# Optimization experiments

Hardware: AMD Instinct MI355X
Metric: run time of the kernel (lower is better)

Reference implementation:

```python
import jax, jax.numpy as jnp
import numpy as np

N = 50000          # num nodes
E = 800000         # num edges
H, C = 2, 64       # heads, per-head channels (hidden_dim=64)
IN_DIM = 128
EDGE_DIM = 32
NEG_SLOPE = 0.2


def setup_inputs() -> dict:
    key = jax.random.key(0)
    ks = jax.random.split(key, 20)
    s = 0.05
    inp = {
        'x': jax.random.normal(ks[0], (N, IN_DIM), jnp.float32),
        'edge_index': jax.random.randint(ks[1], (2, E), 0, N, jnp.int64),
        'edge_attr': jax.random.normal(ks[2], (E, EDGE_DIM), jnp.float32),
    }
    k = 3
    for l in range(3):
        inp[f'Wl{l}'] = jax.random.normal(ks[k], (IN_DIM, H * C), jnp.float32) * s; k += 1
        inp[f'Wr{l}'] = jax.random.normal(ks[k], (IN_DIM, H * C), jnp.float32) * s; k += 1
        inp[f'We{l}'] = jax.random.normal(ks[k], (EDGE_DIM, H * C), jnp.float32) * s; k += 1
        inp[f'att{l}'] = jax.random.normal(ks[k], (H, C), jnp.float32) * s; k += 1
        inp[f'b{l}'] = jnp.zeros((H * C,), jnp.float32)
    return inp


def gatv2_layer(x, src, dst, edge_attr, Wl, Wr, We, att, b):
    # PyG GATv2Conv (concat=True, share_weights=False):
    #   e_ij = att . LeakyReLU(Wl x_j + Wr x_i + We edge_ij)
    #   alpha = softmax_j over neighborhood of dst i; out_i = sum_j alpha_ij * (Wl x_j)
    xl = (x @ Wl).reshape(-1, H, C)              # [N,H,C] source transform
    xr = (x @ Wr).reshape(-1, H, C)              # [N,H,C] target transform
    ea = (edge_attr @ We).reshape(-1, H, C)      # [E,H,C]
    xj = xl[src]                                 # [E,H,C] gather source
    e = jax.nn.leaky_relu(xj + xr[dst] + ea, NEG_SLOPE)
    logits = jnp.einsum('ehc,hc->eh', e, att)    # [E,H]
    # segment softmax over dst neighborhoods
    m = jax.ops.segment_max(logits, dst, num_segments=N)  # [N,H]
    m = jnp.where(jnp.isfinite(m), m, 0.0)
    ex = jnp.exp(logits - m[dst])
    denom = jax.ops.segment_sum(ex, dst, num_segments=N)  # [N,H]
    alpha = ex / (denom[dst] + 1e-16)            # [E,H]
    out = jax.ops.segment_sum(alpha[:, :, None] * xj, dst, num_segments=N)  # [N,H,C]
    return out.reshape(-1, H * C) + b


def reference(x, edge_index, edge_attr,
              Wl0, Wr0, We0, att0, b0,
              Wl1, Wr1, We1, att1, b1,
              Wl2, Wr2, We2, att2, b2):
    src, dst = edge_index[0], edge_index[1]
    h = gatv2_layer(x, src, dst, edge_attr, Wl0, Wr0, We0, att0, b0)
    h = jax.nn.relu(h)
    h = gatv2_layer(h, src, dst, edge_attr, Wl1, Wr1, We1, att1, b1)
    h = jax.nn.relu(h)
    h = gatv2_layer(h, src, dst, edge_attr, Wl2, Wr2, We2, att2, b2)
    return h
```

## Files before the change

### kernel.cpp

```cpp
#include <hip/hip_runtime.h>

typedef unsigned int u32;
typedef unsigned short u16;
typedef __attribute__((ext_vector_type(8))) short bf16x8;
typedef __attribute__((ext_vector_type(4))) float f32x4;

__device__ __forceinline__ u16 f2b(float f){
  u32 x = __float_as_uint(f);
  u32 r = (x + 0x7fffu + ((x >> 16) & 1u)) >> 16;
  return (u16)r;
}
__device__ __forceinline__ float b2f(u16 h){ return __uint_as_float((u32)h << 16); }
__device__ __forceinline__ float bl(u32 u){ return __uint_as_float(u << 16); }
__device__ __forceinline__ float bh(u32 u){ return __uint_as_float(u & 0xffff0000u); }


__global__ void k_detect(const u32* __restrict__ ei, int n, u32* __restrict__ flag){
  int t = blockIdx.x * blockDim.x + threadIdx.x;
  u32 v = 0;
  if (t < n) v = ei[2 * t + 1];
  unsigned long long b = __ballot(v != 0u);
  if ((threadIdx.x & 63) == 0 && b) atomicOr(flag, 1u);
}

__global__ void k_convhist(const int* __restrict__ ei, int* __restrict__ src, int* __restrict__ dst,
                           int* __restrict__ deg, int E, const u32* __restrict__ flag){
  int e = blockIdx.x * blockDim.x + threadIdx.x;
  if (e >= E) return;
  bool is64 = (*flag == 0u);
  int s, d;
  if (is64){ s = ei[2 * e]; d = ei[2 * (E + e)]; }
  else     { s = ei[e];     d = ei[E + e]; }
  src[e] = s; dst[e] = d;
  atomicAdd(&deg[d], 1);
}

__global__ __launch_bounds__(256) void k_scan1(const int* __restrict__ deg, int* __restrict__ bsum, int n,
                                               int* __restrict__ ssrc, int* __restrict__ sdst,
                                               u16* __restrict__ ea2s_pad, int E){
  int b = blockIdx.x, t = threadIdx.x, lane = t & 63, wv = t >> 6;
  if (b == 0){
    if (t < 64){ ssrc[E + t] = 0; sdst[E + t] = 0; }
    ((uint4*)ea2s_pad)[t] = make_uint4(0, 0, 0, 0);
  }
  int i0 = b * 1024 + t * 4;
  int4 v = make_int4(0,0,0,0);
  if (i0 + 3 < n) v = *(const int4*)(deg + i0);
  else { if (i0 < n) v.x = deg[i0]; if (i0+1 < n) v.y = deg[i0+1]; if (i0+2 < n) v.z = deg[i0+2]; }
  int s = v.x + v.y + v.z + v.w;
  #pragma unroll
  for (int off = 1; off < 64; off <<= 1) s += __shfl_xor(s, off);
  __shared__ int ws[4];
  if (lane == 0) ws[wv] = s;
  __syncthreads();
  if (t == 0) bsum[b] = ws[0] + ws[1] + ws[2] + ws[3];
}

__global__ __launch_bounds__(1024) void k_scan2(int* __restrict__ bsum, int nb, int* __restrict__ segN){
  int t = threadIdx.x, lane = t & 63, w = t >> 6;
  int v = (t < nb) ? bsum[t] : 0;
  int x = v;
  #pragma unroll
  for (int off = 1; off < 64; off <<= 1){
    int y = __shfl_up(x, off);
    if (lane >= off) x += y;
  }
  __shared__ int wsum[16];
  if (lane == 63) wsum[w] = x;
  __syncthreads();
  if (w == 0 && lane < 16){
    int sv = wsum[lane];
    #pragma unroll
    for (int off = 1; off < 16; off <<= 1){
      int y = __shfl_up(sv, off);
      if (lane >= off) sv += y;
    }
    wsum[lane] = sv;
  }
  __syncthreads();
  int woff = (w > 0) ? wsum[w - 1] : 0;
  if (t < nb) bsum[t] = woff + x - v;
  if (t == 0) *segN = wsum[15];
}

__global__ __launch_bounds__(256) void k_scan3(const int* __restrict__ deg, const int* __restrict__ bsum,
                                               int* __restrict__ seg, int n){
  int b = blockIdx.x, t = threadIdx.x, lane = t & 63, wv = t >> 6;
  int i0 = b * 1024 + t * 4;
  int4 v = make_int4(0,0,0,0);
  if (i0 + 3 < n) v = *(const int4*)(deg + i0);
  else { if (i0 < n) v.x = deg[i0]; if (i0+1 < n) v.y = deg[i0+1]; if (i0+2 < n) v.z = deg[i0+2]; }
  int s = v.x + v.y + v.z + v.w;
  int x = s;
  #pragma unroll
  for (int off = 1; off < 64; off <<= 1){
    int y = __shfl_up(x, off);
    if (lane >= off) x += y;
  }
  __shared__ int ws[4];
  if (lane == 63) ws[wv] = x;
  __syncthreads();
  int woff = 0;
  #pragma unroll
  for (int k = 0; k < 4; k++) if (k < wv) woff += ws[k];
  int base = bsum[b] + woff + (x - s);
  if (i0 < n)     seg[i0]     = base;
  if (i0+1 < n)   seg[i0+1]   = base + v.x;
  if (i0+2 < n)   seg[i0+2]   = base + v.x + v.y;
  if (i0+3 < n)   seg[i0+3]   = base + v.x + v.y + v.z;
}

__global__ void k_scatter(const int* __restrict__ src, const int* __restrict__ dst,
                          const int* __restrict__ seg, int* __restrict__ cur,
                          int* __restrict__ ssrc, int* __restrict__ sdst,
                          int* __restrict__ seid, int E){
  int e = blockIdx.x * blockDim.x + threadIdx.x;
  if (e >= E) return;
  int d = dst[e];
  int pos = seg[d] + atomicAdd(&cur[d], 1);
  ssrc[pos] = src[e];
  sdst[pos] = d;
  seid[pos] = e;
}

__global__ void k_sortb(const int* __restrict__ seid, const float* __restrict__ eattr,
                        u16* __restrict__ ea2s, int E){
  int t = blockIdx.x * blockDim.x + threadIdx.x;
  int e = t >> 3, j = t & 7;
  if (e >= E) return;
  int eid = seid[e];
  float4 v = *(const float4*)(eattr + (size_t)eid * 32 + j * 4);
  u32 p0 = (u32)f2b(v.x) | ((u32)f2b(v.y) << 16);
  u32 p1 = (u32)f2b(v.z) | ((u32)f2b(v.w) << 16);
  *(uint2*)(ea2s + (size_t)e * 32 + j * 4) = make_uint2(p0, p1);
}

__global__ __launch_bounds__(256) void k_prepw(
    const float* __restrict__ W0, const float* __restrict__ W1, const float* __restrict__ W2,
    const float* __restrict__ W3, const float* __restrict__ W4, const float* __restrict__ W5,
    u16* __restrict__ WtH, u16* __restrict__ WtL)
{
  int mat = blockIdx.z;
  const float* W = (mat == 0) ? W0 : (mat == 1) ? W1 : (mat == 2) ? W2 :
                   (mat == 3) ? W3 : (mat == 4) ? W4 : W5;
  __shared__ float tile[32][33];
  int kt = blockIdx.x * 32, ct = blockIdx.y * 32;
  int tr = threadIdx.x & 31, ti = threadIdx.x >> 5;
  #pragma unroll
  for (int j = 0; j < 4; j++){
    int kk = ti + 8 * j;
    tile[kk][tr] = W[(size_t)(kt + kk) * 128 + ct + tr];
  }
  __syncthreads();
  #pragma unroll
  for (int j = 0; j < 4; j++){
    int cc = ti + 8 * j;
    float v = tile[tr][cc];
    u16 hi = f2b(v);
    u16 lo = f2b(v - b2f(hi));
    size_t o = (size_t)mat * 16384 + (size_t)(ct + cc) * 128 + kt + tr;
    WtH[o] = hi;
    WtL[o] = lo;
  }
}

__global__ __launch_bounds__(512) void k_gemm2(
    const float* __restrict__ A,
    const u16* __restrict__ WtH, const u16* __restrict__ WtL,
    u16* __restrict__ xlb, u16* __restrict__ xrb, int nrows)
{
  __shared__ u16 sAH[64][32], sAL[64][32];
  __shared__ u16 sWH[256][32], sWL[256][32];
  int t = threadIdx.x, wv = t >> 6, lane = t & 63;
  int col = lane & 15, kg = lane >> 4;
  int mat = wv >> 2, cq = wv & 3;
  int r0 = blockIdx.x * 64;

  f32x4 acc[4][2];
  #pragma unroll
  for (int m = 0; m < 4; m++)
    #pragma unroll
    for (int n = 0; n < 2; n++)
      acc[m][n] = (f32x4){0.f, 0.f, 0.f, 0.f};

  int ar = t >> 3, ak = (t & 7) << 2;
  int wmt = t >> 8, wtt = t & 255;
  int wc = wtt >> 1, wk = (wtt & 1) << 4;

  for (int kh = 0; kh < 4; kh++){
    __syncthreads();
    {
      int gr = r0 + ar;
      const float* ap = A + (size_t)gr * 128 + kh * 32 + ak;
      float4 va = {0,0,0,0};
      if (gr < nrows) va = *(const float4*)ap;
      u16 h0 = f2b(va.x), h1 = f2b(va.y), h2 = f2b(va.z), h3 = f2b(va.w);
      u16 l0 = f2b(va.x - b2f(h0)), l1 = f2b(va.y - b2f(h1));
      u16 l2 = f2b(va.z - b2f(h2)), l3 = f2b(va.w - b2f(h3));
      *(uint2*)&sAH[ar][ak] = make_uint2((u32)h0 | ((u32)h1 << 16), (u32)h2 | ((u32)h3 << 16));
      *(uint2*)&sAL[ar][ak] = make_uint2((u32)l0 | ((u32)l1 << 16), (u32)l2 | ((u32)l3 << 16));
    }
    {
      const u16* gh = WtH + (size_t)wmt * 16384 + (size_t)wc * 128 + kh * 32 + wk;
      const u16* gl = WtL + (size_t)wmt * 16384 + (size_t)wc * 128 + kh * 32 + wk;
      uint4 h0 = *(const uint4*)gh, h1 = *(const uint4*)(gh + 8);
      uint4 l0 = *(const uint4*)gl, l1 = *(const uint4*)(gl + 8);
      *(uint4*)&sWH[wmt * 128 + wc][wk]     = h0; *(uint4*)&sWH[wmt * 128 + wc][wk + 8] = h1;
      *(uint4*)&sWL[wmt * 128 + wc][wk]     = l0; *(uint4*)&sWL[wmt * 128 + wc][wk + 8] = l1;
    }
    __syncthreads();
    int wb = mat * 128 + cq * 32;
    bf16x8 bhi0 = *(const bf16x8*)&sWH[wb + col]     [kg*8];
    bf16x8 bhi1 = *(const bf16x8*)&sWH[wb + 16 + col][kg*8];
    bf16x8 blo0 = *(const bf16x8*)&sWL[wb + col]     [kg*8];
    bf16x8 blo1 = *(const bf16x8*)&sWL[wb + 16 + col][kg*8];
    #pragma unroll
    for (int m = 0; m < 4; m++){
      bf16x8 ahv = *(const bf16x8*)&sAH[m*16 + col][kg*8];
      bf16x8 alv = *(const bf16x8*)&sAL[m*16 + col][kg*8];
      acc[m][0] = __builtin_amdgcn_mfma_f32_16x16x32_bf16(ahv, bhi0, acc[m][0], 0, 0, 0);
      acc[m][0] = __builtin_amdgcn_mfma_f32_16x16x32_bf16(alv, bhi0, acc[m][0], 0, 0, 0);
      acc[m][0] = __builtin_amdgcn_mfma_f32_16x16x32_bf16(ahv, blo0, acc[m][0], 0, 0, 0);
      acc[m][1] = __builtin_amdgcn_mfma_f32_16x16x32_bf16(ahv, bhi1, acc[m][1], 0, 0, 0);
      acc[m][1] = __builtin_amdgcn_mfma_f32_16x16x32_bf16(alv, bhi1, acc[m][1], 0, 0, 0);
      acc[m][1] = __builtin_amdgcn_mfma_f32_16x16x32_bf16(ahv, blo1, acc[m][1], 0, 0, 0);
    }
  }
  u16* ob = mat ? xrb : xlb;
  #pragma unroll
  for (int m = 0; m < 4; m++){
    #pragma unroll
    for (int n = 0; n < 2; n++){
      #pragma unroll
      for (int r = 0; r < 4; r++){
        int row = r0 + m*16 + kg*4 + r;
        int c   = cq*32 + n*16 + col;
        if (row < nrows) ob[(size_t)row * 128 + c] = f2b(acc[m][n][r]);
      }
    }
  }
}

__global__ __launch_bounds__(256) void k_edge(
    const int* __restrict__ ssrc, const int* __restrict__ sdst,
    const u16* __restrict__ ea2s,
    const u16* __restrict__ xlb, const u16* __restrict__ xrb,
    const float* __restrict__ We, const float* __restrict__ att,
    float2* __restrict__ pr2, int ntiles, int E)
{
  __shared__ float sD[4][16][132];
  int wv = threadIdx.x >> 6, lane = threadIdx.x & 63;
  int col = lane & 15, kg = lane >> 4;
  int er = lane >> 2, q = lane & 3;

  bf16x8 bw[8];
  #pragma unroll
  for (int c = 0; c < 8; c++)
    #pragma unroll
    for (int j = 0; j < 8; j++)
      bw[c][j] = (short)f2b(We[(kg * 8 + j) * 128 + c * 16 + col]);
  u32 attp[16];
  #pragma unroll
  for (int i = 0; i < 16; i++)
    attp[i] = (u32)f2b(att[q * 32 + 2*i]) | ((u32)f2b(att[q * 32 + 2*i + 1]) << 16);

  int nw = gridDim.x * 4;
  int t = blockIdx.x * 4 + wv;
  if (t >= ntiles) return;

  int e0 = t * 16;
  int p = e0 + er;
  bf16x8 aA = *(const bf16x8*)(ea2s + (size_t)(e0 + col) * 32 + kg * 8);
  int snA = ssrc[p], dnA = sdst[p];
  const u16* xjA = xlb + (size_t)snA * 128 + q * 32;
  uint4 jA0 = ((const uint4*)xjA)[0], jA1 = ((const uint4*)xjA)[1],
        jA2 = ((const uint4*)xjA)[2], jA3 = ((const uint4*)xjA)[3];

  int tB = t + nw;
  int tBc = (tB < ntiles) ? tB : t;
  int eB = tBc * 16;
  int pB = eB + er;
  bf16x8 aB = *(const bf16x8*)(ea2s + (size_t)(eB + col) * 32 + kg * 8);
  int snB = ssrc[pB], dnB = sdst[pB];
  const u16* xjB = xlb + (size_t)snB * 128 + q * 32;
  uint4 jB0 = ((const uint4*)xjB)[0], jB1 = ((const uint4*)xjB)[1],
        jB2 = ((const uint4*)xjB)[2], jB3 = ((const uint4*)xjB)[3];

  while (true){
    const u16* xip = xrb + (size_t)dnA * 128 + q * 32;
    uint4 i0 = ((const uint4*)xip)[0], i1 = ((const uint4*)xip)[1],
          i2 = ((const uint4*)xip)[2], i3 = ((const uint4*)xip)[3];

    int tC = t + 2 * nw;
    int tCc = (tC < ntiles) ? tC : t;
    int eC = tCc * 16;
    int pC = eC + er;
    bf16x8 aC = *(const bf16x8*)(ea2s + (size_t)(eC + col) * 32 + kg * 8);
    int snC = ssrc[pC], dnC = sdst[pC];
    const u16* xjC = xlb + (size_t)snC * 128 + q * 32;
    uint4 jC0 = ((const uint4*)xjC)[0], jC1 = ((const uint4*)xjC)[1],
          jC2 = ((const uint4*)xjC)[2], jC3 = ((const uint4*)xjC)[3];

    #pragma unroll
    for (int c = 0; c < 8; c++){
      f32x4 d = __builtin_amdgcn_mfma_f32_16x16x32_bf16(aA, bw[c], (f32x4){0.f,0.f,0.f,0.f}, 0, 0, 0);
      #pragma unroll
      for (int r = 0; r < 4; r++)
        sD[wv][kg * 4 + r][c * 16 + col] = d[r];
    }

    const float* drow = &sD[wv][er][q * 32];
    float acc = 0.f;
#define EPK(KO, JQ, IQ) { \
    float4 d0 = *(const float4*)(drow + KO*8); \
    float4 d1 = *(const float4*)(drow + KO*8 + 4); \
    float v; u32 jw, iw, aw; \
    jw = JQ.x; iw = IQ.x; aw = attp[KO*4+0]; \
    v = d0.x + bl(jw) + bl(iw); v = fmaxf(v, 0.2f*v); acc = fmaf(v, bl(aw), acc); \
    v = d0.y + bh(jw) + bh(iw); v = fmaxf(v, 0.2f*v); acc = fmaf(v, bh(aw), acc); \
    jw = JQ.y; iw = IQ.y; aw = attp[KO*4+1]; \
    v = d0.z + bl(jw) + bl(iw); v = fmaxf(v, 0.2f*v); acc = fmaf(v, bl(aw), acc); \
    v = d0.w + bh(jw) + bh(iw); v = fmaxf(v, 0.2f*v); acc = fmaf(v, bh(aw), acc); \
    jw = JQ.z; iw = IQ.z; aw = attp[KO*4+2]; \
    v = d1.x + bl(jw) + bl(iw); v = fmaxf(v, 0.2f*v); acc = fmaf(v, bl(aw), acc); \
    v = d1.y + bh(jw) + bh(iw); v = fmaxf(v, 0.2f*v); acc = fmaf(v, bh(aw), acc); \
    jw = JQ.w; iw = IQ.w; aw = attp[KO*4+3]; \
    v = d1.z + bl(jw) + bl(iw); v = fmaxf(v, 0.2f*v); acc = fmaf(v, bl(aw), acc); \
    v = d1.w + bh(jw) + bh(iw); v = fmaxf(v, 0.2f*v); acc = fmaf(v, bh(aw), acc); }
    EPK(0, jA0, i0) EPK(1, jA1, i1) EPK(2, jA2, i2) EPK(3, jA3, i3)
#undef EPK
    acc += __shfl_xor(acc, 1);
    float other = __shfl_xor(acc, 2);
    if (q == 0 && p < E){
      pr2[p] = make_float2(__expf(fminf(acc, 80.f)), __expf(fminf(other, 80.f)));
    }
    int t2 = t + nw;
    if (t2 >= ntiles) break;
    t = t2; p = pB;
    aA = aB; dnA = dnB;
    jA0 = jB0; jA1 = jB1; jA2 = jB2; jA3 = jB3;
    aB = aC; dnB = dnC; pB = pC;
    jB0 = jC0; jB1 = jC1; jB2 = jC2; jB3 = jC3;
  }
}

template<int RELU>
__global__ __launch_bounds__(256) void k_seg2(
    const int* __restrict__ seg, const int* __restrict__ ssrc,
    const float2* __restrict__ pr2,
    const u16* __restrict__ xlb, const float* __restrict__ bias,
    float* __restrict__ out, int N)
{
  int wid  = blockIdx.x * 4 + (threadIdx.x >> 6);
  int lane = threadIdx.x & 63;
  if (wid >= N) return;
  int eg = lane >> 4, cb = lane & 15, c0 = cb * 8;
  int hsel = cb >> 3;

  int p0 = seg[wid], p1 = seg[wid + 1];
  float s = 0.f;
  float o0 = 0.f, o1 = 0.f, o2 = 0.f, o3 = 0.f, o4 = 0.f, o5 = 0.f, o6 = 0.f, o7 = 0.f;

  if (p0 < p1){
#define LDB(PP, QV, XV) { \
    int ii = PP + eg; ii = (ii < p1) ? ii : (p1 - 1); \
    int sn = ssrc[ii]; \
    QV = pr2[ii]; \
    XV = *(const uint4*)(xlb + (size_t)sn * 128 + c0); }
    int p = p0;
    float2 qa; uint4 xa;
    LDB(p, qa, xa)
    int pBb = p + 4; int pBc = (pBb < p1) ? pBb : p;
    float2 qb; uint4 xb;
    LDB(pBc, qb, xb)
    while (true){
      int pCb = p + 8; int pCc = (pCb < p1) ? pCb : p;
      float2 qc; uint4 xc;
      LDB(pCc, qc, xc)
      float e = hsel ? qa.y : qa.x;
      if (p + eg >= p1) e = 0.f;
      s += e;
      o0 = fmaf(e, bl(xa.x), o0); o1 = fmaf(e, bh(xa.x), o1);
      o2 = fmaf(e, bl(xa.y), o2); o3 = fmaf(e, bh(xa.y), o3);
      o4 = fmaf(e, bl(xa.z), o4); o5 = fmaf(e, bh(xa.z), o5);
      o6 = fmaf(e, bl(xa.w), o6); o7 = fmaf(e, bh(xa.w), o7);
      if (p + 4 >= p1) break;
      p += 4;
      qa = qb; xa = xb;
      qb = qc; xb = xc;
    }
#undef LDB
  }
  s  += __shfl_xor(s, 16);  s  += __shfl_xor(s, 32);
  o0 += __shfl_xor(o0, 16); o0 += __shfl_xor(o0, 32);
  o1 += __shfl_xor(o1, 16); o1 += __shfl_xor(o1, 32);
  o2 += __shfl_xor(o2, 16); o2 += __shfl_xor(o2, 32);
  o3 += __shfl_xor(o3, 16); o3 += __shfl_xor(o3, 32);
  o4 += __shfl_xor(o4, 16); o4 += __shfl_xor(o4, 32);
  o5 += __shfl_xor(o5, 16); o5 += __shfl_xor(o5, 32);
  o6 += __shfl_xor(o6, 16); o6 += __shfl_xor(o6, 32);
  o7 += __shfl_xor(o7, 16); o7 += __shfl_xor(o7, 32);

  if (eg == 0){
    float inv = 1.0f / (s + 1e-16f);
    float4 b0 = *(const float4*)(bias + c0);
    float4 b1 = *(const float4*)(bias + c0 + 4);
    float r0 = fmaf(o0, inv, b0.x), r1 = fmaf(o1, inv, b0.y);
    float r2 = fmaf(o2, inv, b0.z), r3 = fmaf(o3, inv, b0.w);
    float r4 = fmaf(o4, inv, b1.x), r5 = fmaf(o5, inv, b1.y);
    float r6 = fmaf(o6, inv, b1.z), r7 = fmaf(o7, inv, b1.w);
    if (RELU){
      r0 = fmaxf(r0, 0.f); r1 = fmaxf(r1, 0.f); r2 = fmaxf(r2, 0.f); r3 = fmaxf(r3, 0.f);
      r4 = fmaxf(r4, 0.f); r5 = fmaxf(r5, 0.f); r6 = fmaxf(r6, 0.f); r7 = fmaxf(r7, 0.f);
    }
    *(float4*)(out + (size_t)wid * 128 + c0)     = make_float4(r0, r1, r2, r3);
    *(float4*)(out + (size_t)wid * 128 + c0 + 4) = make_float4(r4, r5, r6, r7);
  }
}

extern "C" void kernel_launch(void* const* d_in, const int* in_sizes, int n_in,
                              void* d_out, int out_size, void* d_ws, size_t ws_size,
                              hipStream_t stream)
{
  const float* x     = (const float*)d_in[0];
  const int*   ei    = (const int*)  d_in[1];
  const float* eattr = (const float*)d_in[2];
  const float* Wp[3][5];
  for (int l = 0; l < 3; l++)
    for (int j = 0; j < 5; j++)
      Wp[l][j] = (const float*)d_in[3 + l * 5 + j];

  int N = in_sizes[0] / 128;
  int E = in_sizes[2] / 32;

  char* w = (char*)d_ws;
  auto alloc = [&](size_t bytes) -> char* {
    char* p = w; w += (bytes + 255) & ~(size_t)255; return p;
  };
  float* xr   = (float*)alloc((size_t)N * 128 * 4);
  u16*   xlb  = (u16*)  alloc((size_t)N * 128 * 2);
  u16*   xrb  = (u16*)  alloc((size_t)N * 128 * 2);
  u16*   ea2s = (u16*)  alloc((size_t)(E + 64) * 32 * 2);
  float2* prb = (float2*)alloc((size_t)E * 8);
  u16*   WtH  = (u16*)  alloc((size_t)6 * 16384 * 2);
  u16*   WtL  = (u16*)  alloc((size_t)6 * 16384 * 2);
  int* srcA   = (int*)alloc((size_t)E * 4);
  int* dstA   = (int*)alloc((size_t)E * 4);
  int* ssrc   = (int*)alloc((size_t)(E + 64) * 4);
  int* sdst   = (int*)alloc((size_t)(E + 64) * 4);
  int* seid   = (int*)alloc((size_t)E * 4);
  int* seg    = (int*)alloc((size_t)(N + 1) * 4);
  int* bsum   = (int*)alloc(1024 * 4);
  char* zbase = alloc((size_t)N * 4);      int* deg  = (int*)zbase;
  char* zcur  = alloc((size_t)N * 4);      int* cur  = (int*)zcur;
  char* zflag = alloc(256);                u32* flag = (u32*)zflag;
  size_t zspan = (size_t)(zflag + 256 - zbase);

  hipMemsetAsync(zbase, 0, zspan, stream);

  int ndet = (E < 16384) ? E : 16384;
  k_detect<<<(ndet + 255) / 256, 256, 0, stream>>>((const u32*)ei, ndet, flag);
  int gE = (E + 255) / 256;
  k_convhist<<<gE, 256, 0, stream>>>(ei, srcA, dstA, deg, E, flag);
  int nb = (N + 1023) / 1024;
  k_scan1<<<nb, 256, 0, stream>>>(deg, bsum, N, ssrc, sdst, ea2s + (size_t)E * 32, E);
  k_scan2<<<1, 1024, 0, stream>>>(bsum, nb, seg + N);
  k_scan3<<<nb, 256, 0, stream>>>(deg, bsum, seg, N);
  k_scatter<<<gE, 256, 0, stream>>>(srcA, dstA, seg, cur, ssrc, sdst, seid, E);
  k_sortb<<<(E * 8 + 255) / 256, 256, 0, stream>>>(seid, eattr, ea2s, E);
  dim3 gp(4, 4, 6);
  k_prepw<<<gp, 256, 0, stream>>>(Wp[0][0], Wp[0][1], Wp[1][0], Wp[1][1], Wp[2][0], Wp[2][1], WtH, WtL);

  int gS = (N + 3) / 4;
  int ntiles = (E + 15) / 16;
  int gEdge = (ntiles + 3) / 4; if (gEdge > 2048) gEdge = 2048;
  int gG2 = (N + 63) / 64;

  const float* hin = x;
  for (int l = 0; l < 3; l++){
    k_gemm2<<<gG2, 512, 0, stream>>>(hin, WtH + (size_t)l * 2 * 16384, WtL + (size_t)l * 2 * 16384, xlb, xrb, N);
    k_edge<<<gEdge, 256, 0, stream>>>(ssrc, sdst, ea2s, xlb, xrb, Wp[l][2], Wp[l][3], prb, ntiles, E);
    float* outp = (l == 2) ? (float*)d_out : xr;
    if (l == 2) k_seg2<0><<<gS, 256, 0, stream>>>(seg, ssrc, prb, xlb, Wp[l][4], outp, N);
    else        k_seg2<1><<<gS, 256, 0, stream>>>(seg, ssrc, prb, xlb, Wp[l][4], outp, N);
    hin = xr;
  }
}
```

Before: 466.4 us.

## Process attention heads sequentially in edge kernel with half-size LDS staging

```diff
diff --git a/kernel.cpp b/kernel.cpp
--- a/kernel.cpp
+++ b/kernel.cpp
@@ -248,7 +248,7 @@
     const float* __restrict__ We, const float* __restrict__ att,
     float2* __restrict__ pr2, int ntiles, int E)
 {
-  __shared__ float sD[4][16][132];
+  __shared__ float sDh[4][16][68];
   int wv = threadIdx.x >> 6, lane = threadIdx.x & 63;
   int col = lane & 15, kg = lane >> 4;
   int er = lane >> 2, q = lane & 3;
@@ -261,8 +261,12 @@
       bw[c][j] = (short)f2b(We[(kg * 8 + j) * 128 + c * 16 + col]);
   u32 attp[16];
   #pragma unroll
-  for (int i = 0; i < 16; i++)
-    attp[i] = (u32)f2b(att[q * 32 + 2*i]) | ((u32)f2b(att[q * 32 + 2*i + 1]) << 16);
+  for (int h = 0; h < 2; h++)
+    #pragma unroll
+    for (int i = 0; i < 8; i++){
+      int ch = h * 64 + q * 16 + 2 * i;
+      attp[h * 8 + i] = (u32)f2b(att[ch]) | ((u32)f2b(att[ch + 1]) << 16);
+    }
 
   int nw = gridDim.x * 4;
   int t = blockIdx.x * 4 + wv;
@@ -272,75 +276,86 @@
   int p = e0 + er;
   bf16x8 aA = *(const bf16x8*)(ea2s + (size_t)(e0 + col) * 32 + kg * 8);
   int snA = ssrc[p], dnA = sdst[p];
-  const u16* xjA = xlb + (size_t)snA * 128 + q * 32;
-  uint4 jA0 = ((const uint4*)xjA)[0], jA1 = ((const uint4*)xjA)[1],
-        jA2 = ((const uint4*)xjA)[2], jA3 = ((const uint4*)xjA)[3];
-
-  int tB = t + nw;
-  int tBc = (tB < ntiles) ? tB : t;
-  int eB = tBc * 16;
-  int pB = eB + er;
-  bf16x8 aB = *(const bf16x8*)(ea2s + (size_t)(eB + col) * 32 + kg * 8);
-  int snB = ssrc[pB], dnB = sdst[pB];
-  const u16* xjB = xlb + (size_t)snB * 128 + q * 32;
-  uint4 jB0 = ((const uint4*)xjB)[0], jB1 = ((const uint4*)xjB)[1],
-        jB2 = ((const uint4*)xjB)[2], jB3 = ((const uint4*)xjB)[3];
+  const u16* xjA = xlb + (size_t)snA * 128;
+  uint4 jAa0 = *(const uint4*)(xjA + q * 16),      jAa1 = *(const uint4*)(xjA + q * 16 + 8);
+  uint4 jAb0 = *(const uint4*)(xjA + 64 + q * 16), jAb1 = *(const uint4*)(xjA + 64 + q * 16 + 8);
 
   while (true){
-    const u16* xip = xrb + (size_t)dnA * 128 + q * 32;
-    uint4 i0 = ((const uint4*)xip)[0], i1 = ((const uint4*)xip)[1],
-          i2 = ((const uint4*)xip)[2], i3 = ((const uint4*)xip)[3];
-
-    int tC = t + 2 * nw;
-    int tCc = (tC < ntiles) ? tC : t;
-    int eC = tCc * 16;
-    int pC = eC + er;
-    bf16x8 aC = *(const bf16x8*)(ea2s + (size_t)(eC + col) * 32 + kg * 8);
-    int snC = ssrc[pC], dnC = sdst[pC];
-    const u16* xjC = xlb + (size_t)snC * 128 + q * 32;
-    uint4 jC0 = ((const uint4*)xjC)[0], jC1 = ((const uint4*)xjC)[1],
-          jC2 = ((const uint4*)xjC)[2], jC3 = ((const uint4*)xjC)[3];
-
-    #pragma unroll
-    for (int c = 0; c < 8; c++){
+    const u16* xir = xrb + (size_t)dnA * 128;
+    uint4 iA0 = *(const uint4*)(xir + q * 16), iA1 = *(const uint4*)(xir + q * 16 + 8);
+
+    int t2 = t + nw;
+    bool more = (t2 < ntiles);
+    int tBc = more ? t2 : t;
+    int eB = tBc * 16;
+    int pB = eB + er;
+    bf16x8 aB = *(const bf16x8*)(ea2s + (size_t)(eB + col) * 32 + kg * 8);
+    int snB = ssrc[pB], dnB = sdst[pB];
+    const u16* xjB = xlb + (size_t)snB * 128;
+    uint4 jBa0 = *(const uint4*)(xjB + q * 16),      jBa1 = *(const uint4*)(xjB + q * 16 + 8);
+    uint4 jBb0 = *(const uint4*)(xjB + 64 + q * 16), jBb1 = *(const uint4*)(xjB + 64 + q * 16 + 8);
+
+    #pragma unroll
+    for (int c = 0; c < 4; c++){
       f32x4 d = __builtin_amdgcn_mfma_f32_16x16x32_bf16(aA, bw[c], (f32x4){0.f,0.f,0.f,0.f}, 0, 0, 0);
       #pragma unroll
       for (int r = 0; r < 4; r++)
-        sD[wv][kg * 4 + r][c * 16 + col] = d[r];
-    }
-
-    const float* drow = &sD[wv][er][q * 32];
-    float acc = 0.f;
-#define EPK(KO, JQ, IQ) { \
-    float4 d0 = *(const float4*)(drow + KO*8); \
-    float4 d1 = *(const float4*)(drow + KO*8 + 4); \
-    float v; u32 jw, iw, aw; \
-    jw = JQ.x; iw = IQ.x; aw = attp[KO*4+0]; \
-    v = d0.x + bl(jw) + bl(iw); v = fmaxf(v, 0.2f*v); acc = fmaf(v, bl(aw), acc); \
-    v = d0.y + bh(jw) + bh(iw); v = fmaxf(v, 0.2f*v); acc = fmaf(v, bh(aw), acc); \
-    jw = JQ.y; iw = IQ.y; aw = attp[KO*4+1]; \
-    v = d0.z + bl(jw) + bl(iw); v = fmaxf(v, 0.2f*v); acc = fmaf(v, bl(aw), acc); \
-    v = d0.w + bh(jw) + bh(iw); v = fmaxf(v, 0.2f*v); acc = fmaf(v, bh(aw), acc); \
-    jw = JQ.z; iw = IQ.z; aw = attp[KO*4+2]; \
-    v = d1.x + bl(jw) + bl(iw); v = fmaxf(v, 0.2f*v); acc = fmaf(v, bl(aw), acc); \
-    v = d1.y + bh(jw) + bh(iw); v = fmaxf(v, 0.2f*v); acc = fmaf(v, bh(aw), acc); \
-    jw = JQ.w; iw = IQ.w; aw = attp[KO*4+3]; \
-    v = d1.z + bl(jw) + bl(iw); v = fmaxf(v, 0.2f*v); acc = fmaf(v, bl(aw), acc); \
-    v = d1.w + bh(jw) + bh(iw); v = fmaxf(v, 0.2f*v); acc = fmaf(v, bh(aw), acc); }
-    EPK(0, jA0, i0) EPK(1, jA1, i1) EPK(2, jA2, i2) EPK(3, jA3, i3)
-#undef EPK
-    acc += __shfl_xor(acc, 1);
-    float other = __shfl_xor(acc, 2);
+        sDh[wv][kg * 4 + r][c * 16 + col] = d[r];
+    }
+
+    const float* dr = &sDh[wv][er][q * 16];
+
+#define EPH(J0, J1, I0, I1, AB, ACC) { \
+    float4 d0 = *(const float4*)(dr); \
+    float4 d1 = *(const float4*)(dr + 4); \
+    float4 d2 = *(const float4*)(dr + 8); \
+    float4 d3 = *(const float4*)(dr + 12); \
+    float v; \
+    v = d0.x + bl(J0.x) + bl(I0.x); v = fmaxf(v, 0.2f*v); ACC = fmaf(v, bl(attp[AB+0]), ACC); \
+    v = d0.y + bh(J0.x) + bh(I0.x); v = fmaxf(v, 0.2f*v); ACC = fmaf(v, bh(attp[AB+0]), ACC); \
+    v = d0.z + bl(J0.y) + bl(I0.y); v = fmaxf(v, 0.2f*v); ACC = fmaf(v, bl(attp[AB+1]), ACC); \
+    v = d0.w + bh(J0.y) + bh(I0.y); v = fmaxf(v, 0.2f*v); ACC = fmaf(v, bh(attp[AB+1]), ACC); \
+    v = d1.x + bl(J0.z) + bl(I0.z); v = fmaxf(v, 0.2f*v); ACC = fmaf(v, bl(attp[AB+2]), ACC); \
+    v = d1.y + bh(J0.z) + bh(I0.z); v = fmaxf(v, 0.2f*v); ACC = fmaf(v, bh(attp[AB+2]), ACC); \
+    v = d1.z + bl(J0.w) + bl(I0.w); v = fmaxf(v, 0.2f*v); ACC = fmaf(v, bl(attp[AB+3]), ACC); \
+    v = d1.w + bh(J0.w) + bh(I0.w); v = fmaxf(v, 0.2f*v); ACC = fmaf(v, bh(attp[AB+3]), ACC); \
+    v = d2.x + bl(J1.x) + bl(I1.x); v = fmaxf(v, 0.2f*v); ACC = fmaf(v, bl(attp[AB+4]), ACC); \
+    v = d2.y + bh(J1.x) + bh(I1.x); v = fmaxf(v, 0.2f*v); ACC = fmaf(v, bh(attp[AB+4]), ACC); \
+    v = d2.z + bl(J1.y) + bl(I1.y); v = fmaxf(v, 0.2f*v); ACC = fmaf(v, bl(attp[AB+5]), ACC); \
+    v = d2.w + bh(J1.y) + bh(I1.y); v = fmaxf(v, 0.2f*v); ACC = fmaf(v, bh(attp[AB+5]), ACC); \
+    v = d3.x + bl(J1.z) + bl(I1.z); v = fmaxf(v, 0.2f*v); ACC = fmaf(v, bl(attp[AB+6]), ACC); \
+    v = d3.y + bh(J1.z) + bh(I1.z); v = fmaxf(v, 0.2f*v); ACC = fmaf(v, bh(attp[AB+6]), ACC); \
+    v = d3.z + bl(J1.w) + bl(I1.w); v = fmaxf(v, 0.2f*v); ACC = fmaf(v, bl(attp[AB+7]), ACC); \
+    v = d3.w + bh(J1.w) + bh(I1.w); v = fmaxf(v, 0.2f*v); ACC = fmaf(v, bh(attp[AB+7]), ACC); }
+
+    float hA = 0.f;
+    EPH(jAa0, jAa1, iA0, iA1, 0, hA)
+    hA += __shfl_xor(hA, 1);
+    hA += __shfl_xor(hA, 2);
+
+    uint4 iB0 = *(const uint4*)(xir + 64 + q * 16), iB1 = *(const uint4*)(xir + 64 + q * 16 + 8);
+
+    #pragma unroll
+    for (int c = 4; c < 8; c++){
+      f32x4 d = __builtin_amdgcn_mfma_f32_16x16x32_bf16(aA, bw[c], (f32x4){0.f,0.f,0.f,0.f}, 0, 0, 0);
+      #pragma unroll
+      for (int r = 0; r < 4; r++)
+        sDh[wv][kg * 4 + r][(c - 4) * 16 + col] = d[r];
+    }
+
+    float hB = 0.f;
+    EPH(jAb0, jAb1, iB0, iB1, 8, hB)
+    hB += __shfl_xor(hB, 1);
+    hB += __shfl_xor(hB, 2);
+#undef EPH
+
     if (q == 0 && p < E){
-      pr2[p] = make_float2(__expf(fminf(acc, 80.f)), __expf(fminf(other, 80.f)));
-    }
-    int t2 = t + nw;
-    if (t2 >= ntiles) break;
+      pr2[p] = make_float2(__expf(fminf(hA, 80.f)), __expf(fminf(hB, 80.f)));
+    }
+    if (!more) break;
     t = t2; p = pB;
     aA = aB; dnA = dnB;
-    jA0 = jB0; jA1 = jB1; jA2 = jB2; jA3 = jB3;
-    aB = aC; dnB = dnC; pB = pC;
-    jB0 = jC0; jB1 = jC1; jB2 = jC2; jB3 = jC3;
+    jAa0 = jBa0; jAa1 = jBa1; jAb0 = jBb0; jAb1 = jBb1;
   }
 }
 
```

After: 440.5 us, median of 2. -5.5%, faster.
